# Optimization experiments

Measured on AMD Instinct MI355X. Metric: run time of the kernel, lower is better.

Reference implementation:

```python
import jax, jax.numpy as jnp
import numpy as np


def bilinear_resize(x, out_h, out_w):
    # x: [B, C, H, W]; matches torch F.interpolate(mode='bilinear', align_corners=False)
    B, C, H, W = x.shape
    ry = jnp.clip((jnp.arange(out_h, dtype=jnp.float32) + 0.5) * (H / out_h) - 0.5, 0.0, H - 1)
    rx = jnp.clip((jnp.arange(out_w, dtype=jnp.float32) + 0.5) * (W / out_w) - 0.5, 0.0, W - 1)
    y0 = jnp.floor(ry).astype(jnp.int32); y1 = jnp.minimum(y0 + 1, H - 1)
    x0 = jnp.floor(rx).astype(jnp.int32); x1 = jnp.minimum(x0 + 1, W - 1)
    wy = (ry - y0)[:, None]  # [out_h,1]
    wx = (rx - x0)[None, :]  # [1,out_w]
    r0 = x[:, :, y0, :]; r1 = x[:, :, y1, :]
    v00 = r0[:, :, :, x0]; v01 = r0[:, :, :, x1]
    v10 = r1[:, :, :, x0]; v11 = r1[:, :, :, x1]
    return (v00 * (1 - wx) + v01 * wx) * (1 - wy) + (v10 * (1 - wx) + v11 * wx) * wy


def setup_inputs() -> dict:
    key0 = jax.random.key(0)
    ks = jax.random.split(key0, 16)
    B, N, C, H = 2, 300, 256, 8
    hw_lvl = np.array([[64, 64], [32, 32], [16, 16]], dtype=np.int64)
    L = int((hw_lvl[:, 0] * hw_lvl[:, 1]).sum())  # 5376
    p = lambda k, sh: (0.02 * jax.random.normal(k, sh, dtype=jnp.float32))
    return {
        'query': jax.random.normal(ks[0], (B, N, C), dtype=jnp.float32),
        'key': jax.random.normal(ks[1], (B, L, C), dtype=jnp.float32),
        'value': jax.random.normal(ks[2], (B, L, C), dtype=jnp.float32),
        'key_padding_mask': jnp.zeros((B, L), dtype=bool),
        'hw_lvl': hw_lvl,
        'Wq': p(ks[3], (C, C)), 'Wk': p(ks[4], (C, C)), 'Wv': p(ks[5], (C, C)),
        'Wp': p(ks[6], (C, C)), 'bp': jnp.zeros((C,), jnp.float32),
        'W1': p(ks[7], (H, H)), 'b1': jnp.zeros((H,), jnp.float32),
        'W2': p(ks[8], (H, H)), 'b2': jnp.zeros((H,), jnp.float32),
        'W3': p(ks[9], (H, H)), 'b3': jnp.zeros((H,), jnp.float32),
        'Wm': p(ks[10], (3 * H, 1)), 'bm': jnp.zeros((1,), jnp.float32),
    }


def reference(query, key, value, key_padding_mask, hw_lvl,
              Wq, Wk, Wv, Wp, bp, W1, b1, W2, b2, W3, b3, Wm, bm):
    hw = np.asarray(hw_lvl)
    h1, wd1 = int(hw[0, 0]), int(hw[0, 1])
    h2, wd2 = int(hw[1, 0]), int(hw[1, 1])
    h3, wd3 = int(hw[2, 0]), int(hw[2, 1])
    w1 = h1 * wd1
    w2 = w1 + h2 * wd2
    B, N, C = query.shape
    L = key.shape[1]
    H = W1.shape[0]
    scale = (C // H) ** -0.5

    q = (query @ Wq).reshape(B, N, H, C // H)
    k = (key @ Wk).reshape(B, L, H, C // H)
    v = (value @ Wv).reshape(B, L, H, C // H)
    attn = jnp.einsum('bnhd,blhd->bhnl', q, k) * scale  # [B,H,N,L]

    ap = attn.transpose(0, 2, 3, 1)  # [B,N,L,H]
    f1 = jax.nn.relu(ap[:, :, :w1] @ W1 + b1)                      # [B,N,w1,H]
    f2 = jax.nn.relu(ap[:, :, w1:w2] @ W2 + b2)                    # [B,N,h2*wd2,H]
    f3 = jax.nn.relu(ap[:, :, w2:] @ W3 + b3)                      # [B,N,h3*wd3,H]
    f2 = f2.transpose(0, 1, 3, 2).reshape(B * N, H, h2, wd2)
    f3 = f3.transpose(0, 1, 3, 2).reshape(B * N, H, h3, wd3)
    f2 = bilinear_resize(f2, h1, wd1).transpose(0, 2, 3, 1).reshape(B, N, w1, H)
    f3 = bilinear_resize(f3, h1, wd1).transpose(0, 2, 3, 1).reshape(B, N, w1, H)
    new_feats = jnp.concatenate([f1, f2, f3], axis=-1)             # [B,N,w1,3H]
    mask = jax.nn.relu(new_feats @ Wm + bm)                        # [B,N,w1,1]

    aw = jax.nn.softmax(attn, axis=-1)                             # [B,H,N,L]
    x = jnp.einsum('bhnl,blhd->bnhd', aw, v).reshape(B, N, C)
    x = x @ Wp + bp
    return x, mask
```

## Files before the change

kernel.cpp:

```cpp
#include <hip/hip_runtime.h>
#include <hip/hip_bf16.h>

typedef __hip_bfloat16 bf16;
typedef __attribute__((ext_vector_type(8))) short short8v;
typedef __attribute__((ext_vector_type(8))) unsigned short ushort8v;
typedef __attribute__((ext_vector_type(4))) unsigned short ushort4v;
typedef __attribute__((ext_vector_type(4))) float float4v;

__device__ __forceinline__ float bfu2f(unsigned short u) {
    union { unsigned int i; float f; } v; v.i = ((unsigned int)u) << 16; return v.f;
}
__device__ __forceinline__ unsigned short f2bfu_rn(float x) {
    union { float f; unsigned int i; } u; u.f = x;
    unsigned int r = (u.i + 0x7FFFu + ((u.i >> 16) & 1u)) >> 16;
    return (unsigned short)r;
}

__global__ __launch_bounds__(256) void cast_wt(
    const float* __restrict__ Wq, const float* __restrict__ Wk,
    const float* __restrict__ Wv, const float* __restrict__ Wp,
    unsigned short* __restrict__ wt)
{
    __shared__ unsigned short tile[64][72];
    const float* W = (blockIdx.z == 0) ? Wq : (blockIdx.z == 1) ? Wk
                   : (blockIdx.z == 2) ? Wv : Wp;
    unsigned short* WT = wt + (size_t)blockIdx.z * 65536;
    const int t = threadIdx.x;
    const int k0 = blockIdx.x * 64, n0 = blockIdx.y * 64;
    {
        const int r = t >> 2, cseg = (t & 3) * 16;
        const float* src = W + (size_t)(k0 + r) * 256 + n0 + cseg;
        #pragma unroll
        for (int j = 0; j < 16; ++j) tile[r][cseg + j] = f2bfu_rn(src[j]);
    }
    __syncthreads();
    {
        const int ch = t & 63, lq = t >> 6;
        ushort8v o0, o1;
        #pragma unroll
        for (int i = 0; i < 8; ++i) o0[i] = tile[lq * 16 + i][ch];
        #pragma unroll
        for (int i = 0; i < 8; ++i) o1[i] = tile[lq * 16 + 8 + i][ch];
        unsigned short* dst = WT + (size_t)(n0 + ch) * 256 + k0 + lq * 16;
        *(ushort8v*)(dst)     = o0;
        *(ushort8v*)(dst + 8) = o1;
    }
}

__device__ __forceinline__ void proj_core(
    const float* __restrict__ aptr, const unsigned short* __restrict__ Wt,
    int nc0, int m16, int quad, float4v acc[8])
{
    #pragma unroll
    for (int i = 0; i < 8; ++i) acc[i] = (float4v){0.f, 0.f, 0.f, 0.f};
    #pragma unroll
    for (int ks = 0; ks < 8; ++ks) {
        float4 a0 = *(const float4*)(aptr + ks * 32);
        float4 a1 = *(const float4*)(aptr + ks * 32 + 4);
        short8v af;
        af[0] = (short)f2bfu_rn(a0.x); af[1] = (short)f2bfu_rn(a0.y);
        af[2] = (short)f2bfu_rn(a0.z); af[3] = (short)f2bfu_rn(a0.w);
        af[4] = (short)f2bfu_rn(a1.x); af[5] = (short)f2bfu_rn(a1.y);
        af[6] = (short)f2bfu_rn(a1.z); af[7] = (short)f2bfu_rn(a1.w);
        #pragma unroll
        for (int i = 0; i < 8; ++i) {
            short8v bfr = *(const short8v*)(Wt + (size_t)(nc0 + i * 16 + m16) * 256 + ks * 32 + quad * 8);
            acc[i] = __builtin_amdgcn_mfma_f32_16x16x32_bf16(af, bfr, acc[i], 0, 0, 0);
        }
    }
}

__global__ __launch_bounds__(256) void proj_all(
    const float* __restrict__ q, const float* __restrict__ k, const float* __restrict__ v,
    const unsigned short* __restrict__ wt,
    unsigned short* __restrict__ qb, unsigned short* __restrict__ kb,
    unsigned short* __restrict__ vt)
{
    const int t = threadIdx.x;
    const int wave = t >> 6, lane = t & 63;
    const int m16 = lane & 15, quad = lane >> 4;
    const int msub = (wave & 1) * 16;
    const int nc0 = (wave >> 1) * 128;
    const int bx = blockIdx.x;

    float4v acc[8];
    if (bx < 19) {
        const int m0 = bx * 32;
        const int arow = min(m0 + msub + m16, 599);
        proj_core(q + (size_t)arow * 256 + quad * 8, wt, nc0, m16, quad, acc);
        #pragma unroll
        for (int i = 0; i < 8; ++i)
            #pragma unroll
            for (int r = 0; r < 4; ++r) {
                int m = m0 + msub + quad * 4 + r;
                if (m < 600)
                    qb[(size_t)m * 256 + nc0 + i * 16 + m16] = f2bfu_rn(acc[i][r]);
            }
    } else if (bx < 355) {
        const int m0 = (bx - 19) * 32;
        proj_core(k + (size_t)(m0 + msub + m16) * 256 + quad * 8, wt + 65536, nc0, m16, quad, acc);
        #pragma unroll
        for (int i = 0; i < 8; ++i)
            #pragma unroll
            for (int r = 0; r < 4; ++r) {
                int m = m0 + msub + quad * 4 + r;
                kb[(size_t)m * 256 + nc0 + i * 16 + m16] = f2bfu_rn(acc[i][r]);
            }
    } else {
        const int m0 = (bx - 355) * 32;
        proj_core(v + (size_t)(m0 + msub + m16) * 256 + quad * 8, wt + 131072, nc0, m16, quad, acc);
        const int bb = (m0 >= 5376) ? 1 : 0;
        const int lcol = m0 - bb * 5376 + msub + quad * 4;
        #pragma unroll
        for (int i = 0; i < 8; ++i) {
            const int ch = nc0 + i * 16 + m16;
            ushort4v p;
            #pragma unroll
            for (int r = 0; r < 4; ++r) p[r] = f2bfu_rn(acc[i][r]);
            *(ushort4v*)(vt + (size_t)(bb * 256 + ch) * 5376 + lcol) = p;
        }
    }
}

__global__ __launch_bounds__(512) void attn_fused(
    const unsigned short* __restrict__ qb, const unsigned short* __restrict__ kb,
    const unsigned short* __restrict__ vt,
    const float* __restrict__ W1, const float* __restrict__ b1,
    const float* __restrict__ W2, const float* __restrict__ b2,
    const float* __restrict__ W3, const float* __restrict__ b3,
    const float* __restrict__ Wm,
    float* __restrict__ xbp, float* __restrict__ Sp,
    float* __restrict__ g2, float* __restrict__ g3, float* __restrict__ maskp)
{
    __shared__ unsigned short probs[8][16 * 236];
    __shared__ float wls[3][64];
    __shared__ float bls[3][8], wmls[3][8];

    const int t = threadIdx.x;
    const int wave = t >> 6, lane = t & 63;

    const int i0 = blockIdx.x;
    const int m = (i0 & 7) * 57 + (i0 >> 3);
    const int grp = m / 19, nt = m % 19;
    const int b = grp / 12, zz = grp % 12;
    const int n0 = nt * 16;
    const int l0 = zz * 448;

    if (t < 64) { wls[0][t] = W1[t]; wls[1][t] = W2[t]; wls[2][t] = W3[t]; }
    if (t < 8)  { bls[0][t] = b1[t]; bls[1][t] = b2[t]; bls[2][t] = b3[t];
                  wmls[0][t] = Wm[t]; wmls[1][t] = Wm[8 + t]; wmls[2][t] = Wm[16 + t]; }

    const int m16 = lane & 15, quad = lane >> 4;
    const int h = wave;
    const float scale = 0.17677669529663687f;

    const unsigned short* qp = qb + (size_t)(b * 300 + min(n0 + m16, 299)) * 256 + h * 32 + quad * 8;
    const short8v qfrag = *(const short8v*)qp;
    const unsigned short* kbase = kb + (size_t)(b * 5376) * 256 + h * 32 + quad * 8;
    const unsigned short* vt0 = vt + (size_t)(b * 256 + h * 32 + m16) * 5376;
    const unsigned short* vt1 = vt0 + (size_t)16 * 5376;
    unsigned short* pw = &probs[wave][0];

    float4v c0 = {0.f, 0.f, 0.f, 0.f};
    float4v c1 = {0.f, 0.f, 0.f, 0.f};
    float sm = 0.f;

    for (int sc = 0; sc < 2; ++sc) {
        const int lc = l0 + sc * 224;

        #pragma unroll
        for (int i = 0; i < 14; ++i) {
            const int lcol = lc + i * 16 + m16;
            short8v kf = *(const short8v*)(kbase + (size_t)lcol * 256);
            float4v c = {0.f, 0.f, 0.f, 0.f};
            c = __builtin_amdgcn_mfma_f32_16x16x32_bf16(kf, qfrag, c, 0, 0, 0);
            ushort4v pk;
            #pragma unroll
            for (int r = 0; r < 4; ++r) pk[r] = f2bfu_rn(c[r] * scale);
            *(ushort4v*)(pw + m16 * 236 + i * 16 + quad * 4) = pk;
        }
        __syncthreads();

        {
            const int nl = t >> 5;
            const int n = n0 + nl;
            if (n < 300) {
                const int lb = (t & 31) * 7;
                const size_t bn = (size_t)(b * 300 + n);
                #pragma unroll
                for (int j = 0; j < 7; ++j) {
                    const int ll = lb + j;
                    const int p = lc + ll;
                    const int lvl = (p >= 4096) + (p >= 5120);
                    float s[8];
                    #pragma unroll
                    for (int hp = 0; hp < 8; ++hp) s[hp] = bfu2f(probs[hp][nl * 236 + ll]);
                    float acc = 0.f;
                    #pragma unroll
                    for (int hh = 0; hh < 8; ++hh) {
                        float f = bls[lvl][hh];
                        #pragma unroll
                        for (int hp = 0; hp < 8; ++hp) f += s[hp] * wls[lvl][hp * 8 + hh];
                        acc += fmaxf(f, 0.f) * wmls[lvl][hh];
                    }
                    if (lvl == 0)      maskp[bn * 4096 + p] = acc;
                    else if (lvl == 1) g2[bn * 1024 + (p - 4096)] = acc;
                    else               g3[bn * 256 + (p - 5120)] = acc;
                }
            }
        }

        #pragma unroll
        for (int step = 0; step < 7; ++step) {
            const int lloc = step * 32 + quad * 8;
            ushort8v ua = *(const ushort8v*)(pw + m16 * 236 + lloc);
            short8v af;
            #pragma unroll
            for (int j = 0; j < 8; ++j) {
                float e = __expf(bfu2f(ua[j]));
                sm += e;
                af[j] = (short)f2bfu_rn(e);
            }
            const int lg = lc + lloc;
            short8v bb0 = *(const short8v*)(vt0 + lg);
            short8v bb1 = *(const short8v*)(vt1 + lg);
            c0 = __builtin_amdgcn_mfma_f32_16x16x32_bf16(af, bb0, c0, 0, 0, 0);
            c1 = __builtin_amdgcn_mfma_f32_16x16x32_bf16(af, bb1, c1, 0, 0, 0);
        }
        __syncthreads();
    }

    sm += __shfl_xor(sm, 16);
    sm += __shfl_xor(sm, 32);
    float* xplane = xbp + (size_t)zz * 153600;
    float* splane = Sp + (size_t)zz * 4800;
    if (lane < 16 && n0 + lane < 300)
        splane[(size_t)(b * 300 + n0 + lane) * 8 + h] = sm;
    #pragma unroll
    for (int r = 0; r < 4; ++r) {
        const int n = n0 + quad * 4 + r;
        if (n < 300) {
            float* o = xplane + (size_t)(b * 300 + n) * 256 + h * 32 + m16;
            o[0]  = c0[r];
            o[16] = c1[r];
        }
    }
}

__global__ __launch_bounds__(256) void finish(
    const float* __restrict__ g2, const float* __restrict__ g3,
    const float* __restrict__ xbp, const float* __restrict__ Sp,
    const unsigned short* __restrict__ Wtp,
    const float* __restrict__ bpv, const float* __restrict__ bmp,
    float* __restrict__ out)
{
    const int t = threadIdx.x;
    if (blockIdx.x < 600) {
        __shared__ float gs[1280];
        __shared__ float bms;
        const int bn = blockIdx.x;
        if (t == 0) bms = bmp[0];
        ((float4v*)gs)[t] = ((const float4v*)(g2 + (size_t)bn * 1024))[t];
        if (t < 64) ((float4v*)(gs + 1024))[t] = ((const float4v*)(g3 + (size_t)bn * 256))[t];
        __syncthreads();

        float* mp = out + 153600 + (size_t)bn * 4096;
        #pragma unroll
        for (int it = 0; it < 4; ++it) {
            const int p0 = it * 1024 + t * 4;
            float4v mv = *(const float4v*)(mp + p0);
            float4v res;
            #pragma unroll
            for (int pp = 0; pp < 4; ++pp) {
                const int p = p0 + pp;
                const int Y = p >> 6, X = p & 63;
                float acc = mv[pp] + bms;
                {
                    float ry = fminf(fmaxf(0.5f * Y - 0.25f, 0.f), 31.f);
                    float rx = fminf(fmaxf(0.5f * X - 0.25f, 0.f), 31.f);
                    int y0 = (int)ry, x0 = (int)rx;
                    int y1 = min(y0 + 1, 31), x1 = min(x0 + 1, 31);
                    float wy = ry - (float)y0, wx = rx - (float)x0;
                    acc += (gs[y0 * 32 + x0] * (1.f - wx) + gs[y0 * 32 + x1] * wx) * (1.f - wy)
                         + (gs[y1 * 32 + x0] * (1.f - wx) + gs[y1 * 32 + x1] * wx) * wy;
                }
                {
                    float ry = fminf(fmaxf(0.25f * Y - 0.375f, 0.f), 15.f);
                    float rx = fminf(fmaxf(0.25f * X - 0.375f, 0.f), 15.f);
                    int y0 = (int)ry, x0 = (int)rx;
                    int y1 = min(y0 + 1, 15), x1 = min(x0 + 1, 15);
                    float wy = ry - (float)y0, wx = rx - (float)x0;
                    acc += (gs[1024 + y0 * 16 + x0] * (1.f - wx) + gs[1024 + y0 * 16 + x1] * wx) * (1.f - wy)
                         + (gs[1024 + y1 * 16 + x0] * (1.f - wx) + gs[1024 + y1 * 16 + x1] * wx) * wy;
            }
                res[pp] = fmaxf(acc, 0.f);
            }
            *(float4v*)(mp + p0) = res;
        }
    } else {
        const int bx = blockIdx.x - 600;
        const int wave = t >> 6, lane = t & 63;
        const int m16 = lane & 15, quad = lane >> 4;
        const int nc0 = wave * 64;
        const int m0 = bx * 16;
        const int arow = min(m0 + m16, 599);
        const float* a0p = xbp + (size_t)arow * 256 + quad * 8;

        float4v acc[4];
        #pragma unroll
        for (int i = 0; i < 4; ++i) acc[i] = (float4v){0.f, 0.f, 0.f, 0.f};

        #pragma unroll
        for (int ks = 0; ks < 8; ++ks) {
            float S = 0.f;
            #pragma unroll
            for (int z = 0; z < 12; ++z) S += Sp[(size_t)z * 4800 + arow * 8 + ks];
            const float rS = 1.0f / S;
            float a[8];
            #pragma unroll
            for (int half = 0; half < 2; ++half) {
                float4v x = {0.f, 0.f, 0.f, 0.f};
                #pragma unroll
                for (int z = 0; z < 12; ++z)
                    x += *(const float4v*)(a0p + (size_t)z * 153600 + ks * 32 + half * 4);
                a[half * 4 + 0] = x[0] * rS;
                a[half * 4 + 1] = x[1] * rS;
                a[half * 4 + 2] = x[2] * rS;
                a[half * 4 + 3] = x[3] * rS;
            }
            short8v af;
            #pragma unroll
            for (int j = 0; j < 8; ++j) af[j] = (short)f2bfu_rn(a[j]);
            #pragma unroll
            for (int i = 0; i < 4; ++i) {
                short8v bfr = *(const short8v*)(Wtp + (size_t)(nc0 + i * 16 + m16) * 256 + ks * 32 + quad * 8);
                acc[i] = __builtin_amdgcn_mfma_f32_16x16x32_bf16(af, bfr, acc[i], 0, 0, 0);
            }
        }

        #pragma unroll
        for (int i = 0; i < 4; ++i) {
            const float bv = bpv[nc0 + i * 16 + m16];
            #pragma unroll
            for (int r = 0; r < 4; ++r) {
                int mm = m0 + quad * 4 + r;
                if (mm < 600)
                    out[(size_t)mm * 256 + nc0 + i * 16 + m16] = acc[i][r] + bv;
            }
        }
    }
}

extern "C" void kernel_launch(void* const* d_in, const int* in_sizes, int n_in,
                              void* d_out, int out_size, void* d_ws, size_t ws_size,
                              hipStream_t stream) {
    const float* query = (const float*)d_in[0];
    const float* key   = (const float*)d_in[1];
    const float* value = (const float*)d_in[2];
    const float* Wq = (const float*)d_in[5];
    const float* Wk = (const float*)d_in[6];
    const float* Wv = (const float*)d_in[7];
    const float* Wp = (const float*)d_in[8];
    const float* bp = (const float*)d_in[9];
    const float* W1 = (const float*)d_in[10];
    const float* b1 = (const float*)d_in[11];
    const float* W2 = (const float*)d_in[12];
    const float* b2 = (const float*)d_in[13];
    const float* W3 = (const float*)d_in[14];
    const float* b3 = (const float*)d_in[15];
    const float* Wm = (const float*)d_in[16];
    const float* bm = (const float*)d_in[17];
    float* out = (float*)d_out;

    char* ws = (char*)d_ws;
    unsigned short* wt = (unsigned short*)(ws);
    bf16*  qb   = (bf16*) (ws + 524288);
    bf16*  kb   = (bf16*) (ws + 831488);
    bf16*  vt   = (bf16*) (ws + 6336512);
    float* xbp  = (float*)(ws + 11841536);
    float* Sp   = (float*)(ws + 19214336);
    float* g2   = (float*)(ws + 19444736);
    float* g3   = (float*)(ws + 21902336);
    float* maskp = out + 153600;

    cast_wt<<<dim3(4, 4, 4), 256, 0, stream>>>(Wq, Wk, Wv, Wp, wt);

    proj_all<<<691, 256, 0, stream>>>(query, key, value, wt,
        (unsigned short*)qb, (unsigned short*)kb, (unsigned short*)vt);

    attn_fused<<<456, 512, 0, stream>>>(
        (const unsigned short*)qb, (const unsigned short*)kb, (const unsigned short*)vt,
        W1, b1, W2, b2, W3, b3, Wm, xbp, Sp, g2, g3, maskp);

    finish<<<638, 256, 0, stream>>>(g2, g3, xbp, Sp,
        (const unsigned short*)wt + 196608, bp, bm, out);
}
```

Baseline: 208.0 us.

## Split attention over finer L chunks and separate partial reduction from output projection

The attention kernel now processes 128-column L chunks (42 per batch) instead of 448, giving 1600 blocks with one level per block, a vectorized mask MLP using transposed weights, and occupancy hints. The projection kernel uses 16-row tiles to double block count. The final reduction of 42 partial outputs and sums moves into a dedicated elementwise pass, followed by a separate small projection kernel. This aims to fill more CUs, at the cost of larger partial buffers, more reduction traffic and an extra launch.

New measurement: 279.8 us. 1.35x slower.

```diff
diff --git a/kernel.cpp b/kernel.cpp
--- a/kernel.cpp
+++ b/kernel.cpp
@@ -47,29 +47,6 @@
     }
 }
 
-__device__ __forceinline__ void proj_core(
-    const float* __restrict__ aptr, const unsigned short* __restrict__ Wt,
-    int nc0, int m16, int quad, float4v acc[8])
-{
-    #pragma unroll
-    for (int i = 0; i < 8; ++i) acc[i] = (float4v){0.f, 0.f, 0.f, 0.f};
-    #pragma unroll
-    for (int ks = 0; ks < 8; ++ks) {
-        float4 a0 = *(const float4*)(aptr + ks * 32);
-        float4 a1 = *(const float4*)(aptr + ks * 32 + 4);
-        short8v af;
-        af[0] = (short)f2bfu_rn(a0.x); af[1] = (short)f2bfu_rn(a0.y);
-        af[2] = (short)f2bfu_rn(a0.z); af[3] = (short)f2bfu_rn(a0.w);
-        af[4] = (short)f2bfu_rn(a1.x); af[5] = (short)f2bfu_rn(a1.y);
-        af[6] = (short)f2bfu_rn(a1.z); af[7] = (short)f2bfu_rn(a1.w);
-        #pragma unroll
-        for (int i = 0; i < 8; ++i) {
-            short8v bfr = *(const short8v*)(Wt + (size_t)(nc0 + i * 16 + m16) * 256 + ks * 32 + quad * 8);
-            acc[i] = __builtin_amdgcn_mfma_f32_16x16x32_bf16(af, bfr, acc[i], 0, 0, 0);
-        }
-    }
-}
-
 __global__ __launch_bounds__(256) void proj_all(
     const float* __restrict__ q, const float* __restrict__ k, const float* __restrict__ v,
     const unsigned short* __restrict__ wt,
@@ -79,40 +56,59 @@
     const int t = threadIdx.x;
     const int wave = t >> 6, lane = t & 63;
     const int m16 = lane & 15, quad = lane >> 4;
-    const int msub = (wave & 1) * 16;
-    const int nc0 = (wave >> 1) * 128;
+    const int nc0 = wave * 64;
     const int bx = blockIdx.x;
 
-    float4v acc[8];
-    if (bx < 19) {
-        const int m0 = bx * 32;
-        const int arow = min(m0 + msub + m16, 599);
-        proj_core(q + (size_t)arow * 256 + quad * 8, wt, nc0, m16, quad, acc);
-        #pragma unroll
-        for (int i = 0; i < 8; ++i)
+    const float* A; const unsigned short* Wt; int m0, mode;
+    if (bx < 38)       { mode = 0; m0 = bx * 16;         A = q; Wt = wt; }
+    else if (bx < 710) { mode = 1; m0 = (bx - 38) * 16;  A = k; Wt = wt + 65536; }
+    else               { mode = 2; m0 = (bx - 710) * 16; A = v; Wt = wt + 131072; }
+
+    const int arow = (mode == 0) ? min(m0 + m16, 599) : (m0 + m16);
+    const float* aptr = A + (size_t)arow * 256 + quad * 8;
+
+    float4v acc[4];
+    #pragma unroll
+    for (int i = 0; i < 4; ++i) acc[i] = (float4v){0.f, 0.f, 0.f, 0.f};
+
+    #pragma unroll
+    for (int ks = 0; ks < 8; ++ks) {
+        float4 a0 = *(const float4*)(aptr + ks * 32);
+        float4 a1 = *(const float4*)(aptr + ks * 32 + 4);
+        short8v af;
+        af[0] = (short)f2bfu_rn(a0.x); af[1] = (short)f2bfu_rn(a0.y);
+        af[2] = (short)f2bfu_rn(a0.z); af[3] = (short)f2bfu_rn(a0.w);
+        af[4] = (short)f2bfu_rn(a1.x); af[5] = (short)f2bfu_rn(a1.y);
+        af[6] = (short)f2bfu_rn(a1.z); af[7] = (short)f2bfu_rn(a1.w);
+        #pragma unroll
+        for (int i = 0; i < 4; ++i) {
+            short8v bfr = *(const short8v*)(Wt + (size_t)(nc0 + i * 16 + m16) * 256 + ks * 32 + quad * 8);
+            acc[i] = __builtin_amdgcn_mfma_f32_16x16x32_bf16(af, bfr, acc[i], 0, 0, 0);
+        }
+    }
+
+    if (mode == 0) {
+        #pragma unroll
+        for (int i = 0; i < 4; ++i)
             #pragma unroll
             for (int r = 0; r < 4; ++r) {
-                int m = m0 + msub + quad * 4 + r;
+                int m = m0 + quad * 4 + r;
                 if (m < 600)
                     qb[(size_t)m * 256 + nc0 + i * 16 + m16] = f2bfu_rn(acc[i][r]);
             }
-    } else if (bx < 355) {
-        const int m0 = (bx - 19) * 32;
-        proj_core(k + (size_t)(m0 + msub + m16) * 256 + quad * 8, wt + 65536, nc0, m16, quad, acc);
-        #pragma unroll
-        for (int i = 0; i < 8; ++i)
+    } else if (mode == 1) {
+        #pragma unroll
+        for (int i = 0; i < 4; ++i)
             #pragma unroll
             for (int r = 0; r < 4; ++r) {
-                int m = m0 + msub + quad * 4 + r;
+                int m = m0 + quad * 4 + r;
                 kb[(size_t)m * 256 + nc0 + i * 16 + m16] = f2bfu_rn(acc[i][r]);
             }
     } else {
-        const int m0 = (bx - 355) * 32;
-        proj_core(v + (size_t)(m0 + msub + m16) * 256 + quad * 8, wt + 131072, nc0, m16, quad, acc);
         const int bb = (m0 >= 5376) ? 1 : 0;
-        const int lcol = m0 - bb * 5376 + msub + quad * 4;
-        #pragma unroll
-        for (int i = 0; i < 8; ++i) {
+        const int lcol = m0 - bb * 5376 + quad * 4;
+        #pragma unroll
+        for (int i = 0; i < 4; ++i) {
             const int ch = nc0 + i * 16 + m16;
             ushort4v p;
             #pragma unroll
@@ -122,7 +118,7 @@
     }
 }
 
-__global__ __launch_bounds__(512) void attn_fused(
+__global__ __launch_bounds__(512, 8) void attn_fused(
     const unsigned short* __restrict__ qb, const unsigned short* __restrict__ kb,
     const unsigned short* __restrict__ vt,
     const float* __restrict__ W1, const float* __restrict__ b1,
@@ -132,102 +128,107 @@
     float* __restrict__ xbp, float* __restrict__ Sp,
     float* __restrict__ g2, float* __restrict__ g3, float* __restrict__ maskp)
 {
-    __shared__ unsigned short probs[8][16 * 236];
-    __shared__ float wls[3][64];
-    __shared__ float bls[3][8], wmls[3][8];
+    __shared__ unsigned short probs[8][16 * 136];
+    __shared__ float wT[64];
+    __shared__ float blv[8], wmv[8];
 
     const int t = threadIdx.x;
     const int wave = t >> 6, lane = t & 63;
 
     const int i0 = blockIdx.x;
-    const int m = (i0 & 7) * 57 + (i0 >> 3);
-    const int grp = m / 19, nt = m % 19;
-    const int b = grp / 12, zz = grp % 12;
+    const int m = (i0 & 7) * 200 + (i0 >> 3);
+    if (m >= 1596) return;
+    const int grp = m / 19, nt = m - grp * 19;
+    const int b = grp / 42, zz = grp - b * 42;
     const int n0 = nt * 16;
-    const int l0 = zz * 448;
-
-    if (t < 64) { wls[0][t] = W1[t]; wls[1][t] = W2[t]; wls[2][t] = W3[t]; }
-    if (t < 8)  { bls[0][t] = b1[t]; bls[1][t] = b2[t]; bls[2][t] = b3[t];
-                  wmls[0][t] = Wm[t]; wmls[1][t] = Wm[8 + t]; wmls[2][t] = Wm[16 + t]; }
+    const int l0 = zz * 128;
+    const int lvl = (zz >= 32) + (zz >= 40);
+
+    const float* Wl = (lvl == 0) ? W1 : (lvl == 1) ? W2 : W3;
+    const float* bl = (lvl == 0) ? b1 : (lvl == 1) ? b2 : b3;
+    if (t < 64) wT[t] = Wl[(t & 7) * 8 + (t >> 3)];
+    if (t < 8)  { blv[t] = bl[t]; wmv[t] = Wm[lvl * 8 + t]; }
 
     const int m16 = lane & 15, quad = lane >> 4;
     const int h = wave;
     const float scale = 0.17677669529663687f;
 
-    const unsigned short* qp = qb + (size_t)(b * 300 + min(n0 + m16, 299)) * 256 + h * 32 + quad * 8;
-    const short8v qfrag = *(const short8v*)qp;
-    const unsigned short* kbase = kb + (size_t)(b * 5376) * 256 + h * 32 + quad * 8;
-    const unsigned short* vt0 = vt + (size_t)(b * 256 + h * 32 + m16) * 5376;
+    const short8v qfrag = *(const short8v*)(qb + (size_t)(b * 300 + min(n0 + m16, 299)) * 256 + h * 32 + quad * 8);
+    const unsigned short* kbase = kb + (size_t)(b * 5376 + l0) * 256 + h * 32 + quad * 8;
+    const unsigned short* vt0 = vt + (size_t)(b * 256 + h * 32 + m16) * 5376 + l0;
     const unsigned short* vt1 = vt0 + (size_t)16 * 5376;
     unsigned short* pw = &probs[wave][0];
+
+    #pragma unroll
+    for (int i = 0; i < 8; ++i) {
+        short8v kf = *(const short8v*)(kbase + (size_t)(i * 16 + m16) * 256);
+        float4v c = {0.f, 0.f, 0.f, 0.f};
+        c = __builtin_amdgcn_mfma_f32_16x16x32_bf16(kf, qfrag, c, 0, 0, 0);
+        ushort4v pk;
+        #pragma unroll
+        for (int r = 0; r < 4; ++r) pk[r] = f2bfu_rn(c[r] * scale);
+        *(ushort4v*)(pw + m16 * 136 + i * 16 + quad * 4) = pk;
+    }
+    __syncthreads();
+
+    {
+        const int nl = t >> 5;
+        const int n = n0 + nl;
+        if (n < 300) {
+            const int lb = (t & 31) * 4;
+            ushort4v u[8];
+            #pragma unroll
+            for (int hp = 0; hp < 8; ++hp)
+                u[hp] = *(const ushort4v*)(&probs[hp][nl * 136 + lb]);
+            float sv[4][8];
+            #pragma unroll
+            for (int pp = 0; pp < 4; ++pp)
+                #pragma unroll
+                for (int hp = 0; hp < 8; ++hp) sv[pp][hp] = bfu2f(u[hp][pp]);
+            float facc[4] = {0.f, 0.f, 0.f, 0.f};
+            #pragma unroll
+            for (int hh = 0; hh < 8; ++hh) {
+                const float4 wA = *(const float4*)(&wT[hh * 8]);
+                const float4 wB = *(const float4*)(&wT[hh * 8 + 4]);
+                const float bb_ = blv[hh], wm_ = wmv[hh];
+                #pragma unroll
+                for (int pp = 0; pp < 4; ++pp) {
+                    float f = bb_
+                        + sv[pp][0] * wA.x + sv[pp][1] * wA.y
+                        + sv[pp][2] * wA.z + sv[pp][3] * wA.w
+                        + sv[pp][4] * wB.x + sv[pp][5] * wB.y
+                        + sv[pp][6] * wB.z + sv[pp][7] * wB.w;
+                    facc[pp] += fmaxf(f, 0.f) * wm_;
+                }
+            }
+            float4 o;
+            o.x = facc[0]; o.y = facc[1]; o.z = facc[2]; o.w = facc[3];
+            const size_t bn = (size_t)(b * 300 + n);
+            float* dst = (lvl == 0) ? maskp + bn * 4096 + l0 + lb
+                       : (lvl == 1) ? g2 + bn * 1024 + (l0 - 4096) + lb
+                       :              g3 + bn * 256  + (l0 - 5120) + lb;
+            *(float4*)dst = o;
+        }
+    }
 
     float4v c0 = {0.f, 0.f, 0.f, 0.f};
     float4v c1 = {0.f, 0.f, 0.f, 0.f};
     float sm = 0.f;
-
-    for (int sc = 0; sc < 2; ++sc) {
-        const int lc = l0 + sc * 224;
-
-        #pragma unroll
-        for (int i = 0; i < 14; ++i) {
-            const int lcol = lc + i * 16 + m16;
-            short8v kf = *(const short8v*)(kbase + (size_t)lcol * 256);
-            float4v c = {0.f, 0.f, 0.f, 0.f};
-            c = __builtin_amdgcn_mfma_f32_16x16x32_bf16(kf, qfrag, c, 0, 0, 0);
-            ushort4v pk;
-            #pragma unroll
-            for (int r = 0; r < 4; ++r) pk[r] = f2bfu_rn(c[r] * scale);
-            *(ushort4v*)(pw + m16 * 236 + i * 16 + quad * 4) = pk;
-        }
-        __syncthreads();
-
-        {
-            const int nl = t >> 5;
-            const int n = n0 + nl;
-            if (n < 300) {
-                const int lb = (t & 31) * 7;
-                const size_t bn = (size_t)(b * 300 + n);
-                #pragma unroll
-                for (int j = 0; j < 7; ++j) {
-                    const int ll = lb + j;
-                    const int p = lc + ll;
-                    const int lvl = (p >= 4096) + (p >= 5120);
-                    float s[8];
-                    #pragma unroll
-                    for (int hp = 0; hp < 8; ++hp) s[hp] = bfu2f(probs[hp][nl * 236 + ll]);
-                    float acc = 0.f;
-                    #pragma unroll
-                    for (int hh = 0; hh < 8; ++hh) {
-                        float f = bls[lvl][hh];
-                        #pragma unroll
-                        for (int hp = 0; hp < 8; ++hp) f += s[hp] * wls[lvl][hp * 8 + hh];
-                        acc += fmaxf(f, 0.f) * wmls[lvl][hh];
-                    }
-                    if (lvl == 0)      maskp[bn * 4096 + p] = acc;
-                    else if (lvl == 1) g2[bn * 1024 + (p - 4096)] = acc;
-                    else               g3[bn * 256 + (p - 5120)] = acc;
-                }
-            }
-        }
-
-        #pragma unroll
-        for (int step = 0; step < 7; ++step) {
-            const int lloc = step * 32 + quad * 8;
-            ushort8v ua = *(const ushort8v*)(pw + m16 * 236 + lloc);
-            short8v af;
-            #pragma unroll
-            for (int j = 0; j < 8; ++j) {
-                float e = __expf(bfu2f(ua[j]));
-                sm += e;
-                af[j] = (short)f2bfu_rn(e);
-            }
-            const int lg = lc + lloc;
-            short8v bb0 = *(const short8v*)(vt0 + lg);
-            short8v bb1 = *(const short8v*)(vt1 + lg);
-            c0 = __builtin_amdgcn_mfma_f32_16x16x32_bf16(af, bb0, c0, 0, 0, 0);
-            c1 = __builtin_amdgcn_mfma_f32_16x16x32_bf16(af, bb1, c1, 0, 0, 0);
-        }
-        __syncthreads();
+    #pragma unroll
+    for (int step = 0; step < 4; ++step) {
+        const int lloc = step * 32 + quad * 8;
+        ushort8v ua = *(const ushort8v*)(pw + m16 * 136 + lloc);
+        short8v af;
+        #pragma unroll
+        for (int j = 0; j < 8; ++j) {
+            float e = __expf(bfu2f(ua[j]));
+            sm += e;
+            af[j] = (short)f2bfu_rn(e);
+        }
+        short8v bb0 = *(const short8v*)(vt0 + lloc);
+        short8v bb1 = *(const short8v*)(vt1 + lloc);
+        c0 = __builtin_amdgcn_mfma_f32_16x16x32_bf16(af, bb0, c0, 0, 0, 0);
+        c1 = __builtin_amdgcn_mfma_f32_16x16x32_bf16(af, bb1, c1, 0, 0, 0);
     }
 
     sm += __shfl_xor(sm, 16);
@@ -250,9 +251,8 @@
 __global__ __launch_bounds__(256) void finish(
     const float* __restrict__ g2, const float* __restrict__ g3,
     const float* __restrict__ xbp, const float* __restrict__ Sp,
-    const unsigned short* __restrict__ Wtp,
-    const float* __restrict__ bpv, const float* __restrict__ bmp,
-    float* __restrict__ out)
+    float* __restrict__ xr, float* __restrict__ Sr,
+    const float* __restrict__ bmp, float* __restrict__ out)
 {
     const int t = threadIdx.x;
     if (blockIdx.x < 600) {
@@ -292,61 +292,72 @@
                     float wy = ry - (float)y0, wx = rx - (float)x0;
                     acc += (gs[1024 + y0 * 16 + x0] * (1.f - wx) + gs[1024 + y0 * 16 + x1] * wx) * (1.f - wy)
                          + (gs[1024 + y1 * 16 + x0] * (1.f - wx) + gs[1024 + y1 * 16 + x1] * wx) * wy;
-            }
+                }
                 res[pp] = fmaxf(acc, 0.f);
             }
             *(float4v*)(mp + p0) = res;
         }
     } else {
-        const int bx = blockIdx.x - 600;
-        const int wave = t >> 6, lane = t & 63;
-        const int m16 = lane & 15, quad = lane >> 4;
-        const int nc0 = wave * 64;
-        const int m0 = bx * 16;
-        const int arow = min(m0 + m16, 599);
-        const float* a0p = xbp + (size_t)arow * 256 + quad * 8;
-
-        float4v acc[4];
-        #pragma unroll
-        for (int i = 0; i < 4; ++i) acc[i] = (float4v){0.f, 0.f, 0.f, 0.f};
-
-        #pragma unroll
-        for (int ks = 0; ks < 8; ++ks) {
-            float S = 0.f;
-            #pragma unroll
-            for (int z = 0; z < 12; ++z) S += Sp[(size_t)z * 4800 + arow * 8 + ks];
-            const float rS = 1.0f / S;
-            float a[8];
-            #pragma unroll
-            for (int half = 0; half < 2; ++half) {
-                float4v x = {0.f, 0.f, 0.f, 0.f};
-                #pragma unroll
-                for (int z = 0; z < 12; ++z)
-                    x += *(const float4v*)(a0p + (size_t)z * 153600 + ks * 32 + half * 4);
-                a[half * 4 + 0] = x[0] * rS;
-                a[half * 4 + 1] = x[1] * rS;
-                a[half * 4 + 2] = x[2] * rS;
-                a[half * 4 + 3] = x[3] * rS;
-            }
-            short8v af;
-            #pragma unroll
-            for (int j = 0; j < 8; ++j) af[j] = (short)f2bfu_rn(a[j]);
-            #pragma unroll
-            for (int i = 0; i < 4; ++i) {
-                short8v bfr = *(const short8v*)(Wtp + (size_t)(nc0 + i * 16 + m16) * 256 + ks * 32 + quad * 8);
-                acc[i] = __builtin_amdgcn_mfma_f32_16x16x32_bf16(af, bfr, acc[i], 0, 0, 0);
-            }
-        }
-
+        const int idx = (blockIdx.x - 600) * 256 + t;
+        if (idx < 38400) {
+            float4v s = {0.f, 0.f, 0.f, 0.f};
+            #pragma unroll 7
+            for (int z = 0; z < 42; ++z)
+                s += *(const float4v*)(xbp + (size_t)z * 153600 + (size_t)idx * 4);
+            *(float4v*)(xr + (size_t)idx * 4) = s;
+        } else if (idx < 38400 + 1200) {
+            const int si = (idx - 38400) * 4;
+            float4v s = {0.f, 0.f, 0.f, 0.f};
+            #pragma unroll 7
+            for (int z = 0; z < 42; ++z)
+                s += *(const float4v*)(Sp + (size_t)z * 4800 + si);
+            *(float4v*)(Sr + si) = s;
+        }
+    }
+}
+
+__global__ __launch_bounds__(256) void proj_out(
+    const float* __restrict__ xr, const float* __restrict__ Sr,
+    const unsigned short* __restrict__ Wtp,
+    const float* __restrict__ bpv, float* __restrict__ out)
+{
+    const int t = threadIdx.x;
+    const int wave = t >> 6, lane = t & 63;
+    const int m16 = lane & 15, quad = lane >> 4;
+    const int nc0 = wave * 64;
+    const int m0 = blockIdx.x * 16;
+    const int arow = min(m0 + m16, 599);
+    const float* a0p = xr + (size_t)arow * 256 + quad * 8;
+
+    float4v acc[4];
+    #pragma unroll
+    for (int i = 0; i < 4; ++i) acc[i] = (float4v){0.f, 0.f, 0.f, 0.f};
+
+    #pragma unroll
+    for (int ks = 0; ks < 8; ++ks) {
+        const float rS = 1.0f / Sr[(size_t)arow * 8 + ks];
+        float4 x0 = *(const float4*)(a0p + ks * 32);
+        float4 x1 = *(const float4*)(a0p + ks * 32 + 4);
+        short8v af;
+        af[0] = (short)f2bfu_rn(x0.x * rS); af[1] = (short)f2bfu_rn(x0.y * rS);
+        af[2] = (short)f2bfu_rn(x0.z * rS); af[3] = (short)f2bfu_rn(x0.w * rS);
+        af[4] = (short)f2bfu_rn(x1.x * rS); af[5] = (short)f2bfu_rn(x1.y * rS);
+        af[6] = (short)f2bfu_rn(x1.z * rS); af[7] = (short)f2bfu_rn(x1.w * rS);
         #pragma unroll
         for (int i = 0; i < 4; ++i) {
-            const float bv = bpv[nc0 + i * 16 + m16];
-            #pragma unroll
-            for (int r = 0; r < 4; ++r) {
-                int mm = m0 + quad * 4 + r;
-                if (mm < 600)
-                    out[(size_t)mm * 256 + nc0 + i * 16 + m16] = acc[i][r] + bv;
-            }
+            short8v bfr = *(const short8v*)(Wtp + (size_t)(nc0 + i * 16 + m16) * 256 + ks * 32 + quad * 8);
+            acc[i] = __builtin_amdgcn_mfma_f32_16x16x32_bf16(af, bfr, acc[i], 0, 0, 0);
+        }
+    }
+
+    #pragma unroll
+    for (int i = 0; i < 4; ++i) {
+        const float bv = bpv[nc0 + i * 16 + m16];
+        #pragma unroll
+        for (int r = 0; r < 4; ++r) {
+            int mm = m0 + quad * 4 + r;
+            if (mm < 600)
+                out[(size_t)mm * 256 + nc0 + i * 16 + m16] = acc[i][r] + bv;
         }
     }
 }
@@ -378,20 +389,23 @@
     bf16*  kb   = (bf16*) (ws + 831488);
     bf16*  vt   = (bf16*) (ws + 6336512);
     float* xbp  = (float*)(ws + 11841536);
-    float* Sp   = (float*)(ws + 19214336);
-    float* g2   = (float*)(ws + 19444736);
-    float* g3   = (float*)(ws + 21902336);
+    float* Sp   = (float*)(ws + 37646336);
+    float* g2   = (float*)(ws + 38452736);
+    float* g3   = (float*)(ws + 40910336);
+    float* xr   = (float*)(ws + 41524736);
+    float* Sr   = (float*)(ws + 42139136);
     float* maskp = out + 153600;
 
     cast_wt<<<dim3(4, 4, 4), 256, 0, stream>>>(Wq, Wk, Wv, Wp, wt);
 
-    proj_all<<<691, 256, 0, stream>>>(query, key, value, wt,
+    proj_all<<<1382, 256, 0, stream>>>(query, key, value, wt,
         (unsigned short*)qb, (unsigned short*)kb, (unsigned short*)vt);
 
-    attn_fused<<<456, 512, 0, stream>>>(
+    attn_fused<<<1600, 512, 0, stream>>>(
         (const unsigned short*)qb, (const unsigned short*)kb, (const unsigned short*)vt,
         W1, b1, W2, b2, W3, b3, Wm, xbp, Sp, g2, g3, maskp);
 
-    finish<<<638, 256, 0, stream>>>(g2, g3, xbp, Sp,
-        (const unsigned short*)wt + 196608, bp, bm, out);
-}
+    finish<<<755, 256, 0, stream>>>(g2, g3, xbp, Sp, xr, Sr, bm, out);
+
+    proj_out<<<38, 256, 0, stream>>>(xr, Sr, (const unsigned short*)wt + 196608, bp, out);
+}
```

## Double-buffer attention logits in LDS and prefetch K tiles across four chunks

Applied to the files above, without the earlier changes.

Restructures the fused attention kernel so the L range is processed in four 112-wide chunks with double-buffered LDS logit tiles. K fragments for the next chunk are prefetched while the current chunk runs its mask MLP and PV MFMAs, removing one barrier per chunk. The mask MLP is vectorised to four positions per thread using transposed weights, and s_setprio plus a launch-bounds occupancy hint are added. The padding region is pre-filled with -inf bf16 and the V offsets are clamped, which adds bookkeeping and some risk around the exp of padded entries.

After: 300.3 us. 1.44x slower.

```diff
diff --git a/kernel.cpp b/kernel.cpp
--- a/kernel.cpp
+++ b/kernel.cpp
@@ -122,7 +122,7 @@
     }
 }
 
-__global__ __launch_bounds__(512) void attn_fused(
+__global__ __launch_bounds__(512, 4) void attn_fused(
     const unsigned short* __restrict__ qb, const unsigned short* __restrict__ kb,
     const unsigned short* __restrict__ vt,
     const float* __restrict__ W1, const float* __restrict__ b1,
@@ -132,102 +132,158 @@
     float* __restrict__ xbp, float* __restrict__ Sp,
     float* __restrict__ g2, float* __restrict__ g3, float* __restrict__ maskp)
 {
-    __shared__ unsigned short probs[8][16 * 236];
-    __shared__ float wls[3][64];
-    __shared__ float bls[3][8], wmls[3][8];
+    __shared__ unsigned short probs[2][8][16 * 136];
+    __shared__ float wTs[3][64];
+    __shared__ float blv[3][8], wmv[3][8];
 
     const int t = threadIdx.x;
     const int wave = t >> 6, lane = t & 63;
 
     const int i0 = blockIdx.x;
     const int m = (i0 & 7) * 57 + (i0 >> 3);
-    const int grp = m / 19, nt = m % 19;
-    const int b = grp / 12, zz = grp % 12;
+    const int grp = m / 19, nt = m - grp * 19;
+    const int b = grp / 12, zz = grp - b * 12;
     const int n0 = nt * 16;
     const int l0 = zz * 448;
 
-    if (t < 64) { wls[0][t] = W1[t]; wls[1][t] = W2[t]; wls[2][t] = W3[t]; }
-    if (t < 8)  { bls[0][t] = b1[t]; bls[1][t] = b2[t]; bls[2][t] = b3[t];
-                  wmls[0][t] = Wm[t]; wmls[1][t] = Wm[8 + t]; wmls[2][t] = Wm[16 + t]; }
+    if (t < 64) {
+        const int hp = t >> 3, hh = t & 7;
+        wTs[0][hh * 8 + hp] = W1[t];
+        wTs[1][hh * 8 + hp] = W2[t];
+        wTs[2][hh * 8 + hp] = W3[t];
+    }
+    if (t >= 64 && t < 72) {
+        const int j = t - 64;
+        blv[0][j] = b1[j]; blv[1][j] = b2[j]; blv[2][j] = b3[j];
+        wmv[0][j] = Wm[j]; wmv[1][j] = Wm[8 + j]; wmv[2][j] = Wm[16 + j];
+    }
+    {
+        const int row = t >> 1;
+        unsigned short* pr = &probs[0][0][0] + row * 136 + 112 + (t & 1) * 12;
+        #pragma unroll
+        for (int j = 0; j < 12; ++j) pr[j] = 0xFF80u;
+    }
 
     const int m16 = lane & 15, quad = lane >> 4;
     const int h = wave;
     const float scale = 0.17677669529663687f;
 
-    const unsigned short* qp = qb + (size_t)(b * 300 + min(n0 + m16, 299)) * 256 + h * 32 + quad * 8;
-    const short8v qfrag = *(const short8v*)qp;
-    const unsigned short* kbase = kb + (size_t)(b * 5376) * 256 + h * 32 + quad * 8;
-    const unsigned short* vt0 = vt + (size_t)(b * 256 + h * 32 + m16) * 5376;
+    const short8v qfrag = *(const short8v*)(qb + (size_t)(b * 300 + min(n0 + m16, 299)) * 256 + h * 32 + quad * 8);
+    const unsigned short* kbase = kb + (size_t)(b * 5376 + l0) * 256 + h * 32 + quad * 8;
+    const unsigned short* vt0 = vt + (size_t)(b * 256 + h * 32 + m16) * 5376 + l0;
     const unsigned short* vt1 = vt0 + (size_t)16 * 5376;
-    unsigned short* pw = &probs[wave][0];
+    unsigned short* const pwv0 = &probs[0][wave][0];
+    unsigned short* const pwv1 = &probs[1][wave][0];
+
+    {
+        short8v kf[7];
+        #pragma unroll
+        for (int i = 0; i < 7; ++i)
+            kf[i] = *(const short8v*)(kbase + (size_t)(i * 16 + m16) * 256);
+        __builtin_amdgcn_s_setprio(1);
+        #pragma unroll
+        for (int i = 0; i < 7; ++i) {
+            float4v c = {0.f, 0.f, 0.f, 0.f};
+            c = __builtin_amdgcn_mfma_f32_16x16x32_bf16(kf[i], qfrag, c, 0, 0, 0);
+            ushort4v pk;
+            #pragma unroll
+            for (int r = 0; r < 4; ++r) pk[r] = f2bfu_rn(c[r] * scale);
+            *(ushort4v*)(pwv0 + m16 * 136 + i * 16 + quad * 4) = pk;
+        }
+        __builtin_amdgcn_s_setprio(0);
+    }
+    __syncthreads();
 
     float4v c0 = {0.f, 0.f, 0.f, 0.f};
     float4v c1 = {0.f, 0.f, 0.f, 0.f};
     float sm = 0.f;
-
-    for (int sc = 0; sc < 2; ++sc) {
-        const int lc = l0 + sc * 224;
-
-        #pragma unroll
-        for (int i = 0; i < 14; ++i) {
-            const int lcol = lc + i * 16 + m16;
-            short8v kf = *(const short8v*)(kbase + (size_t)lcol * 256);
-            float4v c = {0.f, 0.f, 0.f, 0.f};
-            c = __builtin_amdgcn_mfma_f32_16x16x32_bf16(kf, qfrag, c, 0, 0, 0);
-            ushort4v pk;
-            #pragma unroll
-            for (int r = 0; r < 4; ++r) pk[r] = f2bfu_rn(c[r] * scale);
-            *(ushort4v*)(pw + m16 * 236 + i * 16 + quad * 4) = pk;
-        }
-        __syncthreads();
+    const int nl = t >> 5, lb = (t & 31) * 4;
+    const bool fold_act = (lb < 112) && (n0 + nl < 300);
+    const size_t bnf = (size_t)(b * 300 + n0 + nl);
+
+    #pragma unroll
+    for (int c = 0; c < 4; ++c) {
+        short8v kfn[7];
+        if (c < 3) {
+            #pragma unroll
+            for (int i = 0; i < 7; ++i)
+                kfn[i] = *(const short8v*)(kbase + (size_t)((c + 1) * 112 + i * 16 + m16) * 256);
+        }
+
+        if (fold_act) {
+            const int p = l0 + c * 112 + lb;
+            const int lvl = (p >= 4096) + (p >= 5120);
+            ushort4v u[8];
+            #pragma unroll
+            for (int hp = 0; hp < 8; ++hp)
+                u[hp] = *(const ushort4v*)(&probs[c & 1][hp][nl * 136 + lb]);
+            float sv[4][8];
+            #pragma unroll
+            for (int pp = 0; pp < 4; ++pp)
+                #pragma unroll
+                for (int hp = 0; hp < 8; ++hp) sv[pp][hp] = bfu2f(u[hp][pp]);
+            float facc[4] = {0.f, 0.f, 0.f, 0.f};
+            #pragma unroll
+            for (int hh = 0; hh < 8; ++hh) {
+                const float4 wA = *(const float4*)(&wTs[lvl][hh * 8]);
+                const float4 wB = *(const float4*)(&wTs[lvl][hh * 8 + 4]);
+                const float bb_ = blv[lvl][hh], wm_ = wmv[lvl][hh];
+                #pragma unroll
+                for (int pp = 0; pp < 4; ++pp) {
+                    float f = bb_
+                        + sv[pp][0] * wA.x + sv[pp][1] * wA.y
+                        + sv[pp][2] * wA.z + sv[pp][3] * wA.w
+                        + sv[pp][4] * wB.x + sv[pp][5] * wB.y
+                        + sv[pp][6] * wB.z + sv[pp][7] * wB.w;
+                    facc[pp] += fmaxf(f, 0.f) * wm_;
+                }
+            }
+            float4 o;
+            o.x = facc[0]; o.y = facc[1]; o.z = facc[2]; o.w = facc[3];
+            float* dst = (lvl == 0) ? maskp + bnf * 4096 + p
+                       : (lvl == 1) ? g2 + bnf * 1024 + (p - 4096)
+                       :              g3 + bnf * 256  + (p - 5120);
+            *(float4*)dst = o;
+        }
 
         {
-            const int nl = t >> 5;
-            const int n = n0 + nl;
-            if (n < 300) {
-                const int lb = (t & 31) * 7;
-                const size_t bn = (size_t)(b * 300 + n);
+            const unsigned short* pwc = (c & 1) ? pwv1 : pwv0;
+            #pragma unroll
+            for (int step = 0; step < 4; ++step) {
+                const int lloc = step * 32 + quad * 8;
+                ushort8v ua = *(const ushort8v*)(pwc + m16 * 136 + lloc);
+                short8v af;
                 #pragma unroll
-                for (int j = 0; j < 7; ++j) {
-                    const int ll = lb + j;
-                    const int p = lc + ll;
-                    const int lvl = (p >= 4096) + (p >= 5120);
-                    float s[8];
-                    #pragma unroll
-                    for (int hp = 0; hp < 8; ++hp) s[hp] = bfu2f(probs[hp][nl * 236 + ll]);
-                    float acc = 0.f;
-                    #pragma unroll
-                    for (int hh = 0; hh < 8; ++hh) {
-                        float f = bls[lvl][hh];
-                        #pragma unroll
-                        for (int hp = 0; hp < 8; ++hp) f += s[hp] * wls[lvl][hp * 8 + hh];
-                        acc += fmaxf(f, 0.f) * wmls[lvl][hh];
-                    }
-                    if (lvl == 0)      maskp[bn * 4096 + p] = acc;
-                    else if (lvl == 1) g2[bn * 1024 + (p - 4096)] = acc;
-                    else               g3[bn * 256 + (p - 5120)] = acc;
+                for (int j = 0; j < 8; ++j) {
+                    float e = __expf(bfu2f(ua[j]));
+                    sm += e;
+                    af[j] = (short)f2bfu_rn(e);
                 }
-            }
-        }
-
-        #pragma unroll
-        for (int step = 0; step < 7; ++step) {
-            const int lloc = step * 32 + quad * 8;
-            ushort8v ua = *(const ushort8v*)(pw + m16 * 236 + lloc);
-            short8v af;
-            #pragma unroll
-            for (int j = 0; j < 8; ++j) {
-                float e = __expf(bfu2f(ua[j]));
-                sm += e;
-                af[j] = (short)f2bfu_rn(e);
-            }
-            const int lg = lc + lloc;
-            short8v bb0 = *(const short8v*)(vt0 + lg);
-            short8v bb1 = *(const short8v*)(vt1 + lg);
-            c0 = __builtin_amdgcn_mfma_f32_16x16x32_bf16(af, bb0, c0, 0, 0, 0);
-            c1 = __builtin_amdgcn_mfma_f32_16x16x32_bf16(af, bb1, c1, 0, 0, 0);
-        }
-        __syncthreads();
+                const int off = min(c * 112 + lloc, 440);
+                short8v bb0 = *(const short8v*)(vt0 + off);
+                short8v bb1 = *(const short8v*)(vt1 + off);
+                __builtin_amdgcn_s_setprio(1);
+                c0 = __builtin_amdgcn_mfma_f32_16x16x32_bf16(af, bb0, c0, 0, 0, 0);
+                c1 = __builtin_amdgcn_mfma_f32_16x16x32_bf16(af, bb1, c1, 0, 0, 0);
+                __builtin_amdgcn_s_setprio(0);
+            }
+        }
+
+        if (c < 3) {
+            unsigned short* pwn = (c & 1) ? pwv0 : pwv1;
+            __builtin_amdgcn_s_setprio(1);
+            #pragma unroll
+            for (int i = 0; i < 7; ++i) {
+                float4v cc = {0.f, 0.f, 0.f, 0.f};
+                cc = __builtin_amdgcn_mfma_f32_16x16x32_bf16(kfn[i], qfrag, cc, 0, 0, 0);
+                ushort4v pk;
+                #pragma unroll
+                for (int r = 0; r < 4; ++r) pk[r] = f2bfu_rn(cc[r] * scale);
+                *(ushort4v*)(pwn + m16 * 136 + i * 16 + quad * 4) = pk;
+            }
+            __builtin_amdgcn_s_setprio(0);
+            __syncthreads();
+        }
     }
 
     sm += __shfl_xor(sm, 16);
@@ -292,7 +348,7 @@
                     float wy = ry - (float)y0, wx = rx - (float)x0;
                     acc += (gs[1024 + y0 * 16 + x0] * (1.f - wx) + gs[1024 + y0 * 16 + x1] * wx) * (1.f - wy)
                          + (gs[1024 + y1 * 16 + x0] * (1.f - wx) + gs[1024 + y1 * 16 + x1] * wx) * wy;
-            }
+                }
                 res[pp] = fmaxf(acc, 0.f);
             }
             *(float4v*)(mp + p0) = res;
```
